# Optimization experiments

Hardware: AMD Instinct MI355X
Metric: run time of the kernel (lower is better)

Reference implementation:

```python
import jax, jax.numpy as jnp
import numpy as np

NX = 8192      # spectral grid points
P = 128        # unique population eigenvalue atoms tau
ND = 128       # sample-weight diracs d
C = 0.5        # aspect ratio p/n
N_ITER = 40    # damped fixed-point iterations (replaces per-point scipy minimize)


def setup_inputs() -> dict:
    key = jax.random.key(0)
    k1, k2, k3, k4 = jax.random.split(key, 4)
    tau = jnp.sort(jax.random.uniform(k1, (P,), jnp.float32, minval=0.2, maxval=3.0))
    wt = jax.random.uniform(k2, (P,), jnp.float32, minval=0.5, maxval=1.5)
    wt = wt / wt.sum()
    d = jnp.sort(jax.random.uniform(k3, (ND,), jnp.float32, minval=0.5, maxval=2.0))
    wd = jax.random.uniform(k4, (ND,), jnp.float32, minval=0.5, maxval=1.5)
    wd = wd / wd.sum()
    # sin^2 (Chebyshev-like) quadrature grid on the spectral support, as in WeSpeR_density:
    # xij = ul + (ur-ul)*sin(pi*j/(2*(n+1)))^2
    ul = 0.05
    ur = float(3.0 * 2.0 * (1.0 + np.sqrt(C)) ** 2)  # ~ tau_max*d_max*(1+sqrt(c))^2
    j = jnp.arange(1, NX + 1, dtype=jnp.float32)
    x = ul + (ur - ul) * jnp.sin(np.pi * j / (2.0 * (NX + 1))) ** 2
    return {"x": x, "d": d, "wd": wd, "tau": tau, "wt": wt}


def _solve_m_tilde(x, d, wd, tau, wt, c):
    """Batched damped fixed-point solve of the WeSpeR self-consistent equation.

    Solves, for every grid point x simultaneously (lower half-plane branch
    Im(m_tilde) < 0, matching the a - exp(b)*1j parameterization):
        m_tilde = sum_j wd_j*d_j / (1 + c*d_j * S(m_tilde))
        S(m)    = sum_k wt_k*tau_k / (tau_k*m - x)
    which is exactly the stationarity condition of m_tilde_loss_w.
    """
    xc = x.astype(jnp.complex64)                      # [nx]
    wt_tau = (wt * tau).astype(jnp.complex64)         # [p]
    wd_d = (wd * d).astype(jnp.complex64)             # [nd]
    tau_c = tau.astype(jnp.complex64)
    d_c = d.astype(jnp.complex64)
    cc = jnp.complex64(c)

    def F(m):
        # S: [nx] ; inner arrays are [nx, p] and [nx, nd]
        S = jnp.sum(wt_tau[None, :] / (tau_c[None, :] * m[:, None] - xc[:, None]), axis=1)
        return jnp.sum(wd_d[None, :] / (1.0 + cc * d_c[None, :] * S[:, None]), axis=1)

    def body(m, _):
        mn = F(m)
        # keep the solution on the Im < 0 branch (original uses -exp(b) < 0)
        mn = jax.lax.complex(mn.real, jnp.minimum(mn.imag, jnp.float32(-1e-10)))
        m = 0.5 * m + 0.5 * mn  # damping for stable convergence
        return m, None

    m0 = jax.lax.complex(jnp.full(x.shape, jnp.sum(wd * d), dtype=jnp.float32),
                         -jnp.ones(x.shape, jnp.float32))
    m_tilde, _ = jax.lax.scan(body, m0, None, length=N_ITER)
    return m_tilde, xc


def reference(x, d, wd, tau, wt):
    m_tilde, xc = _solve_m_tilde(x, d, wd, tau, wt, C)
    tau_c = tau.astype(jnp.complex64)
    wt_c = wt.astype(jnp.complex64)
    # Stieltjes transform m(x) = sum_k wt_k / (tau_k*m_tilde - x)   (as in m_X_w)
    m = jnp.sum(wt_c[None, :] / (tau_c[None, :] * m_tilde[:, None] - xc[:, None]), axis=1)
    X = -m_tilde / xc
    f = jnp.abs(m.imag) / np.pi  # limiting spectral density
    return (f, m, X)
```

## Files before the change

kernel.cpp:

```cpp
#include <hip/hip_runtime.h>
#include <math.h>

#pragma clang fp contract(off)

#define NXP   8192
#define GROUP 4
#define CPN   32
#define NITER 40

template <int CTRL>
__device__ __forceinline__ float qxor_add(float v) {
    int s = __builtin_amdgcn_update_dpp(0, __float_as_int(v), CTRL, 0xF, 0xF, true);
    return v + __int_as_float(s);
}
#define RED4(v) do {                         \
    v = qxor_add<0xB1>(v);   \
    v = qxor_add<0x4E>(v);   \
} while (0)

__device__ __forceinline__ float div_ieee(float a, float b) {
    float r = __builtin_amdgcn_rcpf(b);
    float e = __builtin_fmaf(-b, r, 1.0f);
    r = __builtin_fmaf(e, r, r);
    e = __builtin_fmaf(-b, r, 1.0f);
    r = __builtin_fmaf(e, r, r);
    float q = a * r;
    float res = __builtin_fmaf(-b, q, a);
    return __builtin_fmaf(res, r, q);
}

__device__ __forceinline__ void cdiv_nr(float nr, float dr, float di,
                                        float& qr, float& qi) {
    bool sw  = fabsf(di) > fabsf(dr);
    float u  = sw ? di : dr;
    float v  = sw ? dr : di;
    float rat = div_ieee(v, u);
    float w   = v * rat;
    float scl = div_ieee(1.0f, u + w);
    float t1  = nr * rat;
    float qrn = sw ? t1 : nr;
    float qin = sw ? nr : t1;
    qr = qrn * scl;
    qi = -qin * scl;
}

__global__ __launch_bounds__(128) void wesper_kernel(
    const float* __restrict__ x,
    const float* __restrict__ d,
    const float* __restrict__ wd,
    const float* __restrict__ tau,
    const float* __restrict__ wt,
    float* __restrict__ out)
{
#pragma clang fp contract(off)
    const int tid = threadIdx.x;
    const int L   = tid & (GROUP - 1);
    const int gid = blockIdx.x * (blockDim.x / GROUP) + (tid >> 2);

    float tauC[CPN], wttC[CPN], wtC[CPN], cdC[CPN], wddC[CPN];
    #pragma unroll
    for (int t = 0; t < CPN; ++t) {
        int k = L + (t << 2);
        float tk = tau[k], wk = wt[k];
        tauC[t] = tk;
        wttC[t] = wk * tk;
        wtC[t]  = wk;
        float dj = d[k];
        cdC[t]  = 0.5f * dj;
        wddC[t] = wd[k] * dj;
    }
    const float xv = x[gid];

    float rA = 0.0f, rB = 0.0f;
    #pragma unroll
    for (int t = 0; t < 16; ++t) {
        int kA = L + (t << 3);
        int kB = kA + 4;
        float vA = wd[kA] * d[kA];
        float vB = wd[kB] * d[kB];
        rA = (t == 0) ? vA : (rA + vA);
        rB = (t == 0) ? vB : (rB + vB);
    }
    RED4(rA);
    RED4(rB);
    float m0 = rA + rB;

    float mr = m0, mi = -1.0f;

    for (int it = 0; it < NITER; ++it) {
        float sre = 0.0f, sim = 0.0f;
        #pragma unroll
        for (int t = 0; t < CPN; ++t) {
            float dr = tauC[t] * mr - xv;
            float di = tauC[t] * mi;
            float qr, qi;
            cdiv_nr(wttC[t], dr, di, qr, qi);
            sre = (t == 0) ? qr : (sre + qr);
            sim = (t == 0) ? qi : (sim + qi);
        }
        RED4(sre);
        RED4(sim);

        float fre = 0.0f, fim = 0.0f;
        #pragma unroll
        for (int t = 0; t < CPN; ++t) {
            float er = 1.0f + cdC[t] * sre;
            float ei = cdC[t] * sim;
            float qr, qi;
            cdiv_nr(wddC[t], er, ei, qr, qi);
            fre = (t == 0) ? qr : (fre + qr);
            fim = (t == 0) ? qi : (fim + qi);
        }
        RED4(fre);
        RED4(fim);

        float mnre = fre;
        float mnim = fminf(fim, -1e-10f);
        mr = 0.5f * mr + 0.5f * mnre;
        mi = 0.5f * mi + 0.5f * mnim;
    }

    float ore = 0.0f, oim = 0.0f;
    #pragma unroll
    for (int t = 0; t < CPN; ++t) {
        float dr = tauC[t] * mr - xv;
        float di = tauC[t] * mi;
        float qr, qi;
        cdiv_nr(wtC[t], dr, di, qr, qi);
        ore = (t == 0) ? qr : (ore + qr);
        oim = (t == 0) ? qi : (oim + qi);
    }
    RED4(ore);
    RED4(oim);

    if (L == 0) {
        out[gid]           = (float)((double)fabsf(oim) / 3.141592653589793);
        out[NXP + gid]     = ore;
        float scl = div_ieee(1.0f, xv);
        out[2 * NXP + gid] = -mr * scl;
    }
}

extern "C" void kernel_launch(void* const* d_in, const int* in_sizes, int n_in,
                              void* d_out, int out_size, void* d_ws, size_t ws_size,
                              hipStream_t stream) {
    const float* x   = (const float*)d_in[0];
    const float* d   = (const float*)d_in[1];
    const float* wd  = (const float*)d_in[2];
    const float* tau = (const float*)d_in[3];
    const float* wt  = (const float*)d_in[4];
    float* out = (float*)d_out;

    const int pts_per_block = 128 / GROUP;
    const int nblocks = NXP / pts_per_block;
    wesper_kernel<<<nblocks, 128, 0, stream>>>(x, d, wd, tau, wt, out);
}
```

Baseline: 194.5 us.

## Split each grid point across 8 lanes with DPP row-shift pairwise reduction

Doubles the number of lanes cooperating on one grid point from 4 to 8, halving the per-lane atom count and the serial complex-division chain per iteration. Partial terms are stored in arrays and combined with a DPP row-shift pull that pairs lane L with L+4, preserving the original summation order, followed by the 4-lane xor reduce and a broadcast from lane 0. This raises thread count and parallelism per point at the cost of extra cross-lane moves and shuffles each iteration.

```diff
diff --git a/kernel.cpp b/kernel.cpp
--- a/kernel.cpp
+++ b/kernel.cpp
@@ -4,19 +4,22 @@
 #pragma clang fp contract(off)
 
 #define NXP   8192
-#define GROUP 4
-#define CPN   32
+#define GROUP 8
+#define CPN   16
 #define NITER 40
 
 template <int CTRL>
-__device__ __forceinline__ float qxor_add(float v) {
-    int s = __builtin_amdgcn_update_dpp(0, __float_as_int(v), CTRL, 0xF, 0xF, true);
-    return v + __int_as_float(s);
+__device__ __forceinline__ float dpp_mov(float v) {
+    return __int_as_float(__builtin_amdgcn_update_dpp(
+        0, __float_as_int(v), CTRL, 0xF, 0xF, true));
 }
+template <int CTRL>
+__device__ __forceinline__ float qxor_add(float v) { return v + dpp_mov<CTRL>(v); }
 #define RED4(v) do {                         \
     v = qxor_add<0xB1>(v);   \
     v = qxor_add<0x4E>(v);   \
 } while (0)
+#define PULL4(v) dpp_mov<0x104>(v)
 
 __device__ __forceinline__ float div_ieee(float a, float b) {
     float r = __builtin_amdgcn_rcpf(b);
@@ -55,64 +58,74 @@
 #pragma clang fp contract(off)
     const int tid = threadIdx.x;
     const int L   = tid & (GROUP - 1);
-    const int gid = blockIdx.x * (blockDim.x / GROUP) + (tid >> 2);
+    const int gid = blockIdx.x * (blockDim.x / GROUP) + (tid >> 3);
 
     float tauC[CPN], wttC[CPN], wtC[CPN], cdC[CPN], wddC[CPN];
     #pragma unroll
-    for (int t = 0; t < CPN; ++t) {
-        int k = L + (t << 2);
+    for (int s = 0; s < CPN; ++s) {
+        int k = L + (s << 3);
         float tk = tau[k], wk = wt[k];
-        tauC[t] = tk;
-        wttC[t] = wk * tk;
-        wtC[t]  = wk;
+        tauC[s] = tk;
+        wttC[s] = wk * tk;
+        wtC[s]  = wk;
         float dj = d[k];
-        cdC[t]  = 0.5f * dj;
-        wddC[t] = wd[k] * dj;
+        cdC[s]  = 0.5f * dj;
+        wddC[s] = wd[k] * dj;
     }
     const float xv = x[gid];
 
-    float rA = 0.0f, rB = 0.0f;
+    float m0 = 0.0f;
     #pragma unroll
-    for (int t = 0; t < 16; ++t) {
-        int kA = L + (t << 3);
-        int kB = kA + 4;
-        float vA = wd[kA] * d[kA];
-        float vB = wd[kB] * d[kB];
-        rA = (t == 0) ? vA : (rA + vA);
-        rB = (t == 0) ? vB : (rB + vB);
-    }
-    RED4(rA);
-    RED4(rB);
-    float m0 = rA + rB;
+    for (int s = 0; s < CPN; ++s)
+        m0 = (s == 0) ? wddC[s] : (m0 + wddC[s]);
+    RED4(m0);
+    m0 += __shfl_xor(m0, 4, 64);
 
     float mr = m0, mi = -1.0f;
+    float qre[CPN], qim[CPN];
 
     for (int it = 0; it < NITER; ++it) {
+        #pragma unroll
+        for (int s = 0; s < CPN; ++s) {
+            float dr = tauC[s] * mr - xv;
+            float di = tauC[s] * mi;
+            cdiv_nr(wttC[s], dr, di, qre[s], qim[s]);
+        }
         float sre = 0.0f, sim = 0.0f;
         #pragma unroll
-        for (int t = 0; t < CPN; ++t) {
-            float dr = tauC[t] * mr - xv;
-            float di = tauC[t] * mi;
-            float qr, qi;
-            cdiv_nr(wttC[t], dr, di, qr, qi);
-            sre = (t == 0) ? qr : (sre + qr);
-            sim = (t == 0) ? qi : (sim + qi);
+        for (int s = 0; s < CPN; ++s) {
+            float pre = PULL4(qre[s]);
+            float pim = PULL4(qim[s]);
+            sre = (s == 0) ? qre[0] : (sre + qre[s]);
+            sim = (s == 0) ? qim[0] : (sim + qim[s]);
+            sre += pre;
+            sim += pim;
         }
         RED4(sre);
         RED4(sim);
+        sre = __shfl(sre, 0, 8);
+        sim = __shfl(sim, 0, 8);
 
+        #pragma unroll
+        for (int s = 0; s < CPN; ++s) {
+            float er = 1.0f + cdC[s] * sre;
+            float ei = cdC[s] * sim;
+            cdiv_nr(wddC[s], er, ei, qre[s], qim[s]);
+        }
         float fre = 0.0f, fim = 0.0f;
         #pragma unroll
-        for (int t = 0; t < CPN; ++t) {
-            float er = 1.0f + cdC[t] * sre;
-            float ei = cdC[t] * sim;
-            float qr, qi;
-            cdiv_nr(wddC[t], er, ei, qr, qi);
-            fre = (t == 0) ? qr : (fre + qr);
-            fim = (t == 0) ? qi : (fim + qi);
+        for (int s = 0; s < CPN; ++s) {
+            float pre = PULL4(qre[s]);
+            float pim = PULL4(qim[s]);
+            fre = (s == 0) ? qre[0] : (fre + qre[s]);
+            fim = (s == 0) ? qim[0] : (fim + qim[s]);
+            fre += pre;
+            fim += pim;
         }
         RED4(fre);
         RED4(fim);
+        fre = __shfl(fre, 0, 8);
+        fim = __shfl(fim, 0, 8);
 
         float mnre = fre;
         float mnim = fminf(fim, -1e-10f);
@@ -120,15 +133,21 @@
         mi = 0.5f * mi + 0.5f * mnim;
     }
 
+    #pragma unroll
+    for (int s = 0; s < CPN; ++s) {
+        float dr = tauC[s] * mr - xv;
+        float di = tauC[s] * mi;
+        cdiv_nr(wtC[s], dr, di, qre[s], qim[s]);
+    }
     float ore = 0.0f, oim = 0.0f;
     #pragma unroll
-    for (int t = 0; t < CPN; ++t) {
-        float dr = tauC[t] * mr - xv;
-        float di = tauC[t] * mi;
-        float qr, qi;
-        cdiv_nr(wtC[t], dr, di, qr, qi);
-        ore = (t == 0) ? qr : (ore + qr);
-        oim = (t == 0) ? qi : (oim + qi);
+    for (int s = 0; s < CPN; ++s) {
+        float pre = PULL4(qre[s]);
+        float pim = PULL4(qim[s]);
+        ore = (s == 0) ? qre[0] : (ore + qre[s]);
+        oim = (s == 0) ? qim[0] : (oim + qim[s]);
+        ore += pre;
+        oim += pim;
     }
     RED4(ore);
     RED4(oim);
```

New measurement: 208.6 us. +7.2%, slower.
